# Kernel optimization log

Measured on AMD Instinct MI355X. Metric: run time of the kernel, lower is better.

The kernel has to match this reference:

```python
import jax, jax.numpy as jnp
import numpy as np

NUM_HEADS = 12   # H
NUM_TASKS = 4    # T
TOP_K = 2        # capacity_factor


def setup_inputs() -> dict:
    key = jax.random.key(0)
    ks = jax.random.split(key, 4)
    B, N, C = 2, 4100, 768  # N = NUM_TASKS + M, M = 4096
    x = jax.random.normal(ks[0], (B, N, C), dtype=jnp.float32)
    # torch.nn.Linear weights are [out_features, in_features]; y = x @ W.T
    qs_w = jax.random.normal(ks[1], (NUM_TASKS, C, C), dtype=jnp.float32) * 0.02
    kv_w = jax.random.normal(ks[2], (2 * C, C), dtype=jnp.float32) * 0.02
    experts_w = jax.random.normal(ks[3], (NUM_TASKS, C, C), dtype=jnp.float32) * 0.02
    return {"x": x, "qs_w": qs_w, "kv_w": kv_w, "experts_w": experts_w}


def reference(x, qs_w, kv_w, experts_w):
    B, N, C = x.shape
    T, H, K = NUM_TASKS, NUM_HEADS, TOP_K
    d = C // H
    M = N - T
    scale = d ** -0.5

    feature = x[:, T:, :]                                    # [B,M,C]
    kv = (feature @ kv_w.T).reshape(B, M, 2, H, d)
    k = jnp.transpose(kv[:, :, 0], (0, 2, 1, 3))             # [B,H,M,d]
    v = jnp.transpose(kv[:, :, 1], (0, 2, 1, 3))             # [B,H,M,d]

    # per-task q projections on task tokens (qs_w[t] is [out,in])
    q = jnp.einsum('btc,toc->bto', x[:, :T], qs_w)           # [B,T,C]
    q = q.reshape(B, T, H, d).transpose(0, 2, 1, 3)          # [B,H,T,d]

    attn = jnp.einsum('bhtd,bhmd->bhtm', q, k) * scale       # [B,H,T,M]
    topv, topi = jax.lax.top_k(attn, K)                      # [B,H,T,K]
    topw = jax.nn.softmax(topv, axis=-1)                     # softmax over top-k only

    # scatter softmaxed top-k back into dense [B,H,T,M] (indices unique per row)
    oh = jax.nn.one_hot(topi, M, dtype=x.dtype)              # [B,H,T,K,M]
    attn_topk = jnp.einsum('bhtk,bhtkm->bhtm', topw, oh)
    attn_token = jnp.einsum('bhtm,bhmd->bhtd', attn_topk, v)
    attn_token = attn_token.transpose(0, 2, 1, 3).reshape(B, T, C)   # [B,T,C]

    # gather top-k feature rows per head/task, weight, and scatter back
    fm = feature.reshape(B, M, H, d).transpose(0, 2, 1, 3)   # [B,H,M,d]
    feat_topk = jnp.take_along_axis(fm[:, :, None], topi[..., None], axis=3)  # [B,H,T,K,d]
    feat_topk = feat_topk * topw[..., None]
    # scatter to [B,H,T,M,d], then permute(0,2,3,1,4)+reshape -> [B,T,M,C]
    feat_pad = jnp.einsum('bhtkd,bhtkm->btmhd', feat_topk, oh).reshape(B, T, M, C)

    # per-task experts (no bias); einsum('btnc,btnc->bnc') with ones = sum over t
    feature_output = jnp.einsum('btmc,toc->bmo', feat_pad, experts_w)  # [B,M,C]
    token_output = jnp.einsum('btc,toc->bto', attn_token, experts_w)   # [B,T,C]

    return jnp.concatenate([token_output, feature_output], axis=1)     # [B,N,C]
```

## Files before the change

kernel.cpp:

```cpp
#include <hip/hip_runtime.h>
#include <math.h>

#define B_ 2
#define N_ 4100
#define C_ 768
#define T_ 4
#define H_ 12
#define D_ 64
#define M_ 4096
#define S_ 48
#define KS_ 8
#define KC_ 96
#define NJ_ 24
#define MT3_ 64
#define SEG_ 8
#define GRID_ 768
#define SCALE 0.125f

__device__ __forceinline__ bool better(float va, int ia, float vb, int ib) {
  return (va > vb) || (va == vb && ia < ib);
}

__device__ __forceinline__ void merge2(float& v1, int& i1, float& v2, int& i2,
                                       float ov1, int oi1, float ov2, int oi2) {
  if (better(ov1, oi1, v1, i1)) {
    float tv; int ti;
    tv = v1; ti = i1; v1 = ov1; i1 = oi1; ov1 = tv; oi1 = ti;
    tv = v2; ti = i2; v2 = ov2; i2 = oi2; ov2 = tv; oi2 = ti;
  }
  if (better(ov1, oi1, v2, i2)) { v2 = ov1; i2 = oi1; }
}

__global__ __launch_bounds__(256) void qkzero_kernel(const float* __restrict__ x,
    const float* __restrict__ qs_w, const float* __restrict__ kv_w,
    float* __restrict__ qk, float* __restrict__ out) {
  const int blk = blockIdx.x;
  const int tid = threadIdx.x;
  if (blk < B_ * S_) {
    const int h = blk % H_;
    const int t = (blk / H_) % T_;
    const int b = blk / S_;
    const int s = t * H_ + h;
    __shared__ float xs[C_];
    __shared__ float red[256];
    __shared__ float qseg[D_];
    for (int i = tid; i < C_; i += 256) xs[i] = x[((size_t)b * N_ + t) * C_ + i];
    __syncthreads();
    {
      const int j = tid & 63;
      const int pt = tid >> 6;
      const float* wr = qs_w + ((size_t)t * C_ + h * D_ + j) * C_ + pt * 192;
      float a = 0.f;
      for (int c = 0; c < 192; ++c) a += xs[pt * 192 + c] * wr[c];
      red[tid] = a;
    }
    __syncthreads();
    if (tid < 64)
      qseg[tid] = (red[tid] + red[tid + 64] + red[tid + 128] + red[tid + 192]) * SCALE;
    __syncthreads();
    for (int c = tid; c < C_; c += 256) {
      float a = 0.f;
      #pragma unroll 8
      for (int j = 0; j < 64; ++j) a += qseg[j] * kv_w[((size_t)(h * D_ + j)) * C_ + c];
      const int kc = c / KC_;
      const int cr = c - kc * KC_;
      qk[(((size_t)b * KS_ + kc) * NJ_ + (cr >> 2)) * (S_ * 4) + s * 4 + (cr & 3)] = a;
    }
  } else {
    const int zb = blk - B_ * S_;
    const int NV4 = (B_ * N_ * C_) / 4;
    float4 z = make_float4(0.f, 0.f, 0.f, 0.f);
    float4* ov = (float4*)out;
    for (int i = zb * 256 + tid; i < NV4; i += (GRID_ - B_ * S_) * 256) ov[i] = z;
  }
}

__global__ __launch_bounds__(256, 4) void score_kernel(const float* __restrict__ x,
    const float* __restrict__ qk, float* __restrict__ part) {
  const int bm = blockIdx.x & 63;
  const int b = blockIdx.x >> 6;
  const int kc = blockIdx.y;
  const int tid = threadIdx.x;

  __shared__ __align__(16) float fbuf[MT3_][100];

  {
    const char* xb = (const char*)(x + ((size_t)b * N_ + T_ + bm * MT3_) * C_ + kc * KC_);
    #pragma unroll
    for (int i = 0; i < 6; ++i) {
      int g = i * 256 + tid;
      int r = g / NJ_;
      int j = g - r * NJ_;
      *(float4*)&fbuf[r][j * 4] = *(const float4*)(xb + (size_t)r * (C_ * 4) + j * 16);
    }
  }
  __syncthreads();

  const int w = tid >> 6;
  const int lane = tid & 63;
  const int s0 = w * 12;

  float acc[12];
  #pragma unroll
  for (int i = 0; i < 12; ++i) acc[i] = 0.f;

  const float* qp = qk + (((size_t)b * KS_ + kc) * NJ_) * (S_ * 4) + s0 * 4;

  float4 fA = *(const float4*)&fbuf[lane][0];
  float4 qA[12], qB[12];
  #pragma unroll
  for (int si = 0; si < 12; ++si) qA[si] = *(const float4*)(qp + si * 4);

  for (int j = 0; j < NJ_; j += 2) {
    float4 fB = *(const float4*)&fbuf[lane][(j + 1) * 4];
    {
      const float* qn = qp + (size_t)(j + 1) * (S_ * 4);
      #pragma unroll
      for (int si = 0; si < 12; ++si) qB[si] = *(const float4*)(qn + si * 4);
    }
    #pragma unroll
    for (int si = 0; si < 12; ++si)
      acc[si] += fA.x * qA[si].x + fA.y * qA[si].y +
                 fA.z * qA[si].z + fA.w * qA[si].w;
    if (j + 2 < NJ_) {
      fA = *(const float4*)&fbuf[lane][(j + 2) * 4];
      const float* qn = qp + (size_t)(j + 2) * (S_ * 4);
      #pragma unroll
      for (int si = 0; si < 12; ++si) qA[si] = *(const float4*)(qn + si * 4);
    }
    #pragma unroll
    for (int si = 0; si < 12; ++si)
      acc[si] += fB.x * qB[si].x + fB.y * qB[si].y +
                 fB.z * qB[si].z + fB.w * qB[si].w;
  }

  const int m = bm * MT3_ + lane;
  #pragma unroll
  for (int si = 0; si < 12; ++si) {
    int s = s0 + si;
    part[(((size_t)kc * B_ + b) * S_ + s) * M_ + m] = acc[si];
  }
}

__global__ __launch_bounds__(256) void reduce_kernel(const float* __restrict__ part,
                                                     float* __restrict__ cand) {
  const int seg = blockIdx.x & 7;
  const int bs = blockIdx.x >> 3;
  const int tid = threadIdx.x;
  const size_t kstride = (size_t)B_ * S_ * M_;
  const float* p0 = part + (size_t)bs * M_ + seg * 512 + tid * 2;
  float a0 = 0.f, a1 = 0.f;
  #pragma unroll
  for (int kc = 0; kc < KS_; ++kc) {
    float2 v = *(const float2*)(p0 + kc * kstride);
    a0 += v.x; a1 += v.y;
  }
  const int mA = seg * 512 + tid * 2;
  float v1, v2; int i1, i2;
  if (better(a0, mA, a1, mA + 1)) { v1 = a0; i1 = mA; v2 = a1; i2 = mA + 1; }
  else                            { v1 = a1; i1 = mA + 1; v2 = a0; i2 = mA; }
  #pragma unroll
  for (int off = 1; off < 64; off <<= 1) {
    float ov1 = __shfl_xor(v1, off);
    int   oi1 = __shfl_xor(i1, off);
    float ov2 = __shfl_xor(v2, off);
    int   oi2 = __shfl_xor(i2, off);
    merge2(v1, i1, v2, i2, ov1, oi1, ov2, oi2);
  }
  __shared__ float cbuf[4][4];
  const int w = tid >> 6, lane = tid & 63;
  if (lane == 0) {
    cbuf[w][0] = v1; ((int*)cbuf[w])[1] = i1;
    cbuf[w][2] = v2; ((int*)cbuf[w])[3] = i2;
  }
  __syncthreads();
  if (tid == 0) {
    for (int ww = 1; ww < 4; ++ww)
      merge2(v1, i1, v2, i2, cbuf[ww][0], ((int*)cbuf[ww])[1],
             cbuf[ww][2], ((int*)cbuf[ww])[3]);
    ((float4*)cand)[blockIdx.x] =
        make_float4(v1, __int_as_float(i1), v2, __int_as_float(i2));
  }
}

__global__ __launch_bounds__(256) void gather_kernel(const float* __restrict__ x,
    const float* __restrict__ kv_w, const float* __restrict__ experts_w,
    const float* __restrict__ cand, float* __restrict__ out) {
  const int h = blockIdx.x % H_;
  const int t = (blockIdx.x / H_) % T_;
  const int b = blockIdx.x / S_;
  const int tid = threadIdx.x;

  __shared__ float f0[C_], f1[C_], fc[C_], red[256];
  __shared__ float attnh[D_];
  __shared__ float sel[4];

  if (tid < 8) {
    float4 cv = ((const float4*)cand)[blockIdx.x * 8 + tid];
    float v1 = cv.x, v2 = cv.z;
    int i1 = __float_as_int(cv.y), i2 = __float_as_int(cv.w);
    #pragma unroll
    for (int off = 1; off < 8; off <<= 1) {
      float ov1 = __shfl_xor(v1, off);
      int   oi1 = __shfl_xor(i1, off);
      float ov2 = __shfl_xor(v2, off);
      int   oi2 = __shfl_xor(i2, off);
      merge2(v1, i1, v2, i2, ov1, oi1, ov2, oi2);
    }
    if (tid == 0) {
      float w1 = 1.f / (1.f + expf(v2 - v1));
      ((int*)sel)[0] = i1; ((int*)sel)[1] = i2;
      sel[2] = w1; sel[3] = 1.f - w1;
    }
  }
  __syncthreads();
  const int i1 = ((const int*)sel)[0];
  const int i2 = ((const int*)sel)[1];
  const float w1 = sel[2], w2 = sel[3];

  const float* r0 = x + ((size_t)b * N_ + T_ + i1) * C_;
  const float* r1 = x + ((size_t)b * N_ + T_ + i2) * C_;
  for (int i = tid; i < C_; i += 256) {
    float a = r0[i], bb = r1[i];
    f0[i] = a; f1[i] = bb; fc[i] = w1 * a + w2 * bb;
  }
  __syncthreads();

  const int j = tid & 63, pt = tid >> 6;
  {
    const float* kr = kv_w + ((size_t)(C_ + h * D_ + j)) * C_ + pt * 192;
    float a = 0.f;
    for (int c = 0; c < 192; ++c) a += fc[pt * 192 + c] * kr[c];
    red[tid] = a;
  }
  __syncthreads();
  if (tid < 64)
    attnh[tid] = red[tid] + red[tid + 64] + red[tid + 128] + red[tid + 192];
  __syncthreads();

  const size_t ot = ((size_t)b * N_ + t) * C_;
  const size_t o0 = ((size_t)b * N_ + T_ + i1) * C_;
  const size_t o1 = ((size_t)b * N_ + T_ + i2) * C_;
  for (int o = tid; o < C_; o += 256) {
    const float* er = experts_w + ((size_t)t * C_ + o) * C_ + h * D_;
    float at = 0.f, a0 = 0.f, a1 = 0.f;
    #pragma unroll 8
    for (int c = 0; c < D_; ++c) {
      float e = er[c];
      at += e * attnh[c];
      a0 += e * f0[h * D_ + c];
      a1 += e * f1[h * D_ + c];
    }
    atomicAdd(&out[ot + o], at);
    atomicAdd(&out[o0 + o], w1 * a0);
    atomicAdd(&out[o1 + o], w2 * a1);
  }
}

extern "C" void kernel_launch(void* const* d_in, const int* in_sizes, int n_in,
                              void* d_out, int out_size, void* d_ws, size_t ws_size,
                              hipStream_t stream) {
  const float* x         = (const float*)d_in[0];
  const float* qs_w      = (const float*)d_in[1];
  const float* kv_w      = (const float*)d_in[2];
  const float* experts_w = (const float*)d_in[3];
  float* out = (float*)d_out;

  float* ws   = (float*)d_ws;
  float* qk   = ws;
  float* part = qk + (size_t)B_ * S_ * C_;
  float* cand = part + (size_t)KS_ * B_ * S_ * M_;

  hipLaunchKernelGGL(qkzero_kernel, dim3(GRID_),          dim3(256), 0, stream, x, qs_w, kv_w, qk, out);
  hipLaunchKernelGGL(score_kernel,  dim3(B_ * 64, KS_),   dim3(256), 0, stream, x, qk, part);
  hipLaunchKernelGGL(reduce_kernel, dim3(B_ * S_ * SEG_), dim3(256), 0, stream, part, cand);
  hipLaunchKernelGGL(gather_kernel, dim3(B_ * S_),        dim3(256), 0, stream, x, kv_w, experts_w, cand, out);
}
```

Baseline: 166.4 us.

## Stage q in shared memory and register-block two rows per thread in score kernel

The score kernel now loads the q·K projection slice into shared memory instead of streaming it from global memory per thread. Each block covers 128 feature rows, with every thread computing two rows, so each q value is reused twice from registers. The reduction dimension is split into 12 chunks of 64 instead of 8 of 96, and qk is written in a plain row-major layout. In exchange, the partial-sum buffer and the reduce kernel's reads grow by half, register pressure rises (launch bound lowered to 3 blocks per SM), and the workspace must hold the larger buffer.

```diff
diff --git a/kernel.cpp b/kernel.cpp
--- a/kernel.cpp
+++ b/kernel.cpp
@@ -9,10 +9,10 @@
 #define D_ 64
 #define M_ 4096
 #define S_ 48
-#define KS_ 8
-#define KC_ 96
-#define NJ_ 24
-#define MT3_ 64
+#define KS_ 12
+#define KC_ 64
+#define NJ_ 16
+#define MT_ 128
 #define SEG_ 8
 #define GRID_ 768
 #define SCALE 0.125f
@@ -40,7 +40,6 @@
     const int h = blk % H_;
     const int t = (blk / H_) % T_;
     const int b = blk / S_;
-    const int s = t * H_ + h;
     __shared__ float xs[C_];
     __shared__ float red[256];
     __shared__ float qseg[D_];
@@ -62,9 +61,7 @@
       float a = 0.f;
       #pragma unroll 8
       for (int j = 0; j < 64; ++j) a += qseg[j] * kv_w[((size_t)(h * D_ + j)) * C_ + c];
-      const int kc = c / KC_;
-      const int cr = c - kc * KC_;
-      qk[(((size_t)b * KS_ + kc) * NJ_ + (cr >> 2)) * (S_ * 4) + s * 4 + (cr & 3)] = a;
+      qk[(size_t)blk * C_ + c] = a;
     }
   } else {
     const int zb = blk - B_ * S_;
@@ -75,23 +72,32 @@
   }
 }
 
-__global__ __launch_bounds__(256, 4) void score_kernel(const float* __restrict__ x,
+__global__ __launch_bounds__(256, 3) void score_kernel(const float* __restrict__ x,
     const float* __restrict__ qk, float* __restrict__ part) {
-  const int bm = blockIdx.x & 63;
-  const int b = blockIdx.x >> 6;
+  const int bm = blockIdx.x & 31;
+  const int b = blockIdx.x >> 5;
   const int kc = blockIdx.y;
   const int tid = threadIdx.x;
 
-  __shared__ __align__(16) float fbuf[MT3_][100];
+  __shared__ __align__(16) float fbuf[MT_][68];
+  __shared__ __align__(16) float qbuf[S_][KC_];
 
   {
-    const char* xb = (const char*)(x + ((size_t)b * N_ + T_ + bm * MT3_) * C_ + kc * KC_);
-    #pragma unroll
-    for (int i = 0; i < 6; ++i) {
+    const char* xb = (const char*)(x + ((size_t)b * N_ + T_ + bm * MT_) * C_ + kc * KC_);
+    #pragma unroll
+    for (int i = 0; i < 8; ++i) {
       int g = i * 256 + tid;
-      int r = g / NJ_;
-      int j = g - r * NJ_;
+      int r = g >> 4, j = g & 15;
       *(float4*)&fbuf[r][j * 4] = *(const float4*)(xb + (size_t)r * (C_ * 4) + j * 16);
+    }
+  }
+  {
+    const char* qb = (const char*)(qk + (size_t)b * S_ * C_ + kc * KC_);
+    #pragma unroll
+    for (int i = 0; i < 3; ++i) {
+      int g = i * 256 + tid;
+      int s = g >> 4, j = g & 15;
+      *(float4*)&qbuf[s][j * 4] = *(const float4*)(qb + (size_t)s * (C_ * 4) + j * 16);
     }
   }
   __syncthreads();
@@ -100,45 +106,53 @@
   const int lane = tid & 63;
   const int s0 = w * 12;
 
-  float acc[12];
-  #pragma unroll
-  for (int i = 0; i < 12; ++i) acc[i] = 0.f;
-
-  const float* qp = qk + (((size_t)b * KS_ + kc) * NJ_) * (S_ * 4) + s0 * 4;
-
-  float4 fA = *(const float4*)&fbuf[lane][0];
-  float4 qA[12], qB[12];
-  #pragma unroll
-  for (int si = 0; si < 12; ++si) qA[si] = *(const float4*)(qp + si * 4);
+  float acc[24];
+  #pragma unroll
+  for (int i = 0; i < 24; ++i) acc[i] = 0.f;
+
+  float4 fA0 = *(const float4*)&fbuf[lane][0];
+  float4 fA1 = *(const float4*)&fbuf[lane + 64][0];
+  float4 qA[12];
+  #pragma unroll
+  for (int si = 0; si < 12; ++si) qA[si] = *(const float4*)&qbuf[s0 + si][0];
 
   for (int j = 0; j < NJ_; j += 2) {
-    float4 fB = *(const float4*)&fbuf[lane][(j + 1) * 4];
-    {
-      const float* qn = qp + (size_t)(j + 1) * (S_ * 4);
+    float4 fB0 = *(const float4*)&fbuf[lane][(j + 1) * 4];
+    float4 fB1 = *(const float4*)&fbuf[lane + 64][(j + 1) * 4];
+    float4 qB[12];
+    #pragma unroll
+    for (int si = 0; si < 12; ++si)
+      qB[si] = *(const float4*)&qbuf[s0 + si][(j + 1) * 4];
+    #pragma unroll
+    for (int si = 0; si < 12; ++si) {
+      acc[si * 2 + 0] += fA0.x * qA[si].x + fA0.y * qA[si].y +
+                         fA0.z * qA[si].z + fA0.w * qA[si].w;
+      acc[si * 2 + 1] += fA1.x * qA[si].x + fA1.y * qA[si].y +
+                         fA1.z * qA[si].z + fA1.w * qA[si].w;
+    }
+    if (j + 2 < NJ_) {
+      fA0 = *(const float4*)&fbuf[lane][(j + 2) * 4];
+      fA1 = *(const float4*)&fbuf[lane + 64][(j + 2) * 4];
       #pragma unroll
-      for (int si = 0; si < 12; ++si) qB[si] = *(const float4*)(qn + si * 4);
-    }
-    #pragma unroll
-    for (int si = 0; si < 12; ++si)
-      acc[si] += fA.x * qA[si].x + fA.y * qA[si].y +
-                 fA.z * qA[si].z + fA.w * qA[si].w;
-    if (j + 2 < NJ_) {
-      fA = *(const float4*)&fbuf[lane][(j + 2) * 4];
-      const float* qn = qp + (size_t)(j + 2) * (S_ * 4);
-      #pragma unroll
-      for (int si = 0; si < 12; ++si) qA[si] = *(const float4*)(qn + si * 4);
-    }
-    #pragma unroll
-    for (int si = 0; si < 12; ++si)
-      acc[si] += fB.x * qB[si].x + fB.y * qB[si].y +
-                 fB.z * qB[si].z + fB.w * qB[si].w;
-  }
-
-  const int m = bm * MT3_ + lane;
+      for (int si = 0; si < 12; ++si)
+        qA[si] = *(const float4*)&qbuf[s0 + si][(j + 2) * 4];
+    }
+    #pragma unroll
+    for (int si = 0; si < 12; ++si) {
+      acc[si * 2 + 0] += fB0.x * qB[si].x + fB0.y * qB[si].y +
+                         fB0.z * qB[si].z + fB0.w * qB[si].w;
+      acc[si * 2 + 1] += fB1.x * qB[si].x + fB1.y * qB[si].y +
+                         fB1.z * qB[si].z + fB1.w * qB[si].w;
+    }
+  }
+
+  const int m0 = bm * MT_;
   #pragma unroll
   for (int si = 0; si < 12; ++si) {
     int s = s0 + si;
-    part[(((size_t)kc * B_ + b) * S_ + s) * M_ + m] = acc[si];
+    float* pp = part + (((size_t)kc * B_ + b) * S_ + s) * M_ + m0 + lane;
+    pp[0]  = acc[si * 2 + 0];
+    pp[64] = acc[si * 2 + 1];
   }
 }
 
@@ -272,7 +286,7 @@
   float* cand = part + (size_t)KS_ * B_ * S_ * M_;
 
   hipLaunchKernelGGL(qkzero_kernel, dim3(GRID_),          dim3(256), 0, stream, x, qs_w, kv_w, qk, out);
-  hipLaunchKernelGGL(score_kernel,  dim3(B_ * 64, KS_),   dim3(256), 0, stream, x, qk, part);
+  hipLaunchKernelGGL(score_kernel,  dim3(B_ * 32, KS_),   dim3(256), 0, stream, x, qk, part);
   hipLaunchKernelGGL(reduce_kernel, dim3(B_ * S_ * SEG_), dim3(256), 0, stream, part, cand);
   hipLaunchKernelGGL(gather_kernel, dim3(B_ * S_),        dim3(256), 0, stream, x, kv_w, experts_w, cand, out);
 }
```

After: 146.4 us. 1.14x faster.
